# Kernel tuning notes

Hardware: AMD Instinct MI355X
Metric: run time of the kernel (lower is better)

Reference implementation:

```python
import jax, jax.numpy as jnp
import numpy as np

E = 262144      # number of edges / neighbors
F = 128         # scalar feature dim
N_RBF = 20      # radial basis functions
RC = 5.0        # cosine cutoff radius


def setup_inputs() -> dict:
    key = jax.random.key(0)
    ks = jax.random.split(key, 9)
    s = jax.random.normal(ks[0], (E, F), dtype=jnp.float32)
    r = jax.random.normal(ks[1], (E, 3), dtype=jnp.float32)   # displacement vectors, |r|~1.7 < RC
    v = jax.random.normal(ks[2], (E, 3, F), dtype=jnp.float32)
    # learned params (fan-in scaled)
    W1 = jax.random.normal(ks[3], (F, F), dtype=jnp.float32) / np.sqrt(F)
    b1 = jnp.zeros((F,), dtype=jnp.float32)
    W2 = jax.random.normal(ks[4], (F, 3 * F), dtype=jnp.float32) / np.sqrt(F)
    b2 = jnp.zeros((3 * F,), dtype=jnp.float32)
    Wr = jax.random.normal(ks[5], (N_RBF, 3 * F), dtype=jnp.float32) / np.sqrt(N_RBF)
    br = jnp.zeros((3 * F,), dtype=jnp.float32)
    return {"s": s, "r": r, "v": v, "W1": W1, "b1": b1, "W2": W2, "b2": b2, "Wr": Wr, "br": br}


def reference(s, r, v, W1, b1, W2, b2, Wr, br):
    # PaiNN message block: RBF/cutoff-gated projections, hadamard splits, sum over edges.
    d = jnp.linalg.norm(r, axis=-1, keepdims=True)                  # [E,1]
    n = jnp.arange(1, N_RBF + 1, dtype=s.dtype)                     # [20]
    rbf = jnp.sin(n * jnp.pi * d / RC) / d                          # [E,20] sinc radial basis
    fcut = 0.5 * (jnp.cos(jnp.pi * d / RC) + 1.0) * (d < RC)        # [E,1] cosine cutoff
    # filter-generating network on scalar features
    phi = jax.nn.silu(s @ W1 + b1) @ W2 + b2                        # [E,384]
    Wfilt = (rbf @ Wr + br) * fcut                                  # [E,384]
    split = Wfilt * phi                                             # [E,384] hadamard gate
    wv1 = split[:, :F]            # gates existing vector features
    ws = split[:, F:2 * F]        # scalar message
    wv2 = split[:, 2 * F:]        # gates unit direction vectors
    out_s = jnp.sum(ws, axis=0)                                     # [128]
    unit_r = r / d                                                  # [E,3]
    dv = unit_r[:, :, None] * wv2[:, None, :] + wv1[:, None, :] * v # [E,3,128]
    out_v = jnp.sum(dv, axis=0)                                     # [3,128]
    return (out_v, out_s)
```

## Files before the change

kernel.cpp:

```cpp
#include <hip/hip_runtime.h>


#define E_TOT  262144
#define NTILES 16384
#define NBLK   256
#define PART_STRIDE 896

typedef __attribute__((ext_vector_type(8))) short bf16x8;
typedef __attribute__((ext_vector_type(4))) float f32x4;
typedef __attribute__((ext_vector_type(4))) unsigned short u16x4;

static __device__ __forceinline__ unsigned short f2bf(float f) {
  union { float f; unsigned u; } x; x.f = f;
  unsigned r = x.u + 0x7fffu + ((x.u >> 16) & 1u);
  return (unsigned short)(r >> 16);
}
static __device__ __forceinline__ float bf2f(unsigned short h) {
  union { unsigned u; float f; } x; x.u = ((unsigned)h) << 16;
  return x.f;
}

#define BAR() do {                                           \
    asm volatile("s_waitcnt lgkmcnt(0)" ::: "memory");       \
    __builtin_amdgcn_s_barrier();                            \
    asm volatile("" ::: "memory");                           \
  } while (0)

__global__ void prep_kernel(const float* __restrict__ W1, const float* __restrict__ W2,
                            const float* __restrict__ Wr,
                            unsigned short* __restrict__ w1t, unsigned short* __restrict__ w2t,
                            unsigned short* __restrict__ wrt) {
  int idx = blockIdx.x * 256 + threadIdx.x;
  if (idx < 16384) {
    int k = idx >> 7, c = idx & 127;
    float x = W1[idx];
    unsigned short hi = f2bf(x);
    w1t[c * 128 + k] = hi;
    w1t[16384 + c * 128 + k] = f2bf(x - bf2f(hi));
  } else if (idx < 65536) {
    int i = idx - 16384;
    int k = i / 384, c = i % 384;
    float x = W2[i];
    unsigned short hi = f2bf(x);
    w2t[c * 128 + k] = hi;
    w2t[49152 + c * 128 + k] = f2bf(x - bf2f(hi));
  } else if (idx < 77824) {
    int i = idx - 65536;
    int c = i >> 5, n = i & 31;
    float x = (n < 20) ? Wr[n * 384 + c] : 0.0f;
    unsigned short hi = f2bf(x);
    wrt[c * 32 + n] = hi;
    wrt[12288 + c * 32 + n] = f2bf(x - bf2f(hi));
  }
}

__global__ __launch_bounds__(512, 2) void painn_main(
    const float* __restrict__ s, const float* __restrict__ r, const float* __restrict__ v,
    const float* __restrict__ b1, const float* __restrict__ b2, const float* __restrict__ br,
    const unsigned short* __restrict__ w1t, const unsigned short* __restrict__ w2t,
    const unsigned short* __restrict__ wrt, float* __restrict__ partials)
{
  __shared__ __align__(16) unsigned short sAh[16][136], sAl[16][136];
  __shared__ __align__(16) unsigned short hAh[16][136], hAl[16][136];
  __shared__ __align__(16) unsigned short rbfh[16][40], rbfl[16][40];
  __shared__ float urA[2][16][9];

  const int tid = threadIdx.x;
  const int wv  = tid >> 6;
  const int ln  = tid & 63;
  const int l15 = ln & 15;
  const int q4  = ln >> 4;

  for (int i = tid; i < 640; i += 512) ((unsigned short*)rbfh)[i] = 0;
  for (int i = tid; i < 640; i += 512) ((unsigned short*)rbfl)[i] = 0;

  const int jh = wv * 16 + l15;
  bf16x8 w1fh[4], w1fl[4];
#pragma unroll
  for (int ks = 0; ks < 4; ++ks) {
    w1fh[ks] = *(const bf16x8*)(w1t + jh * 128 + ks * 32 + q4 * 8);
    w1fl[ks] = *(const bf16x8*)(w1t + 16384 + jh * 128 + ks * 32 + q4 * 8);
  }
  const float b1v = b1[jh];

  const int fcBase = wv * 3;
  int jg[3]; float b2v[3], brv[3];
  bf16x8 w2fh[3][4], w2fl[3][4], wrfh[3], wrfl[3];
#pragma unroll
  for (int fci = 0; fci < 3; ++fci) {
    const int j = (fcBase + fci) * 16 + l15;
    jg[fci] = j;
    b2v[fci] = b2[j];
    brv[fci] = br[j];
#pragma unroll
    for (int ks = 0; ks < 4; ++ks) {
      w2fh[fci][ks] = *(const bf16x8*)(w2t + j * 128 + ks * 32 + q4 * 8);
      w2fl[fci][ks] = *(const bf16x8*)(w2t + 49152 + j * 128 + ks * 32 + q4 * 8);
    }
    wrfh[fci] = *(const bf16x8*)(wrt + j * 32 + q4 * 8);
    wrfl[fci] = *(const bf16x8*)(wrt + 12288 + j * 32 + q4 * 8);
  }

  float accS[3]     = {0.f, 0.f, 0.f};
  float accV1[3][3] = {{0.f,0.f,0.f},{0.f,0.f,0.f},{0.f,0.f,0.f}};
  float accV2[3][3] = {{0.f,0.f,0.f},{0.f,0.f,0.f},{0.f,0.f,0.f}};
  const f32x4 zero4 = {0.f, 0.f, 0.f, 0.f};

  const int srow = tid >> 5;
  const int sc4  = (tid & 31) * 4;
  float4 pf;
  float prx = 0.f, pry = 0.f, prz = 0.f;
  pf = *(const float4*)(s + (size_t)((size_t)blockIdx.x * 16 + srow) * 128 + sc4);
  if (tid < 16) {
    const float* rp = r + ((size_t)blockIdx.x * 16 + tid) * 3;
    prx = rp[0]; pry = rp[1]; prz = rp[2];
  }

  int p = 0;
  for (int t = blockIdx.x; t < NTILES; t += NBLK, p ^= 1) {
    const int e0 = t * 16;

    {
      float xs0 = pf.x, xs1 = pf.y, xs2 = pf.z, xs3 = pf.w;
      u16x4 vh, vl;
      unsigned short h0 = f2bf(xs0); vh[0] = h0; vl[0] = f2bf(xs0 - bf2f(h0));
      unsigned short h1 = f2bf(xs1); vh[1] = h1; vl[1] = f2bf(xs1 - bf2f(h1));
      unsigned short h2 = f2bf(xs2); vh[2] = h2; vl[2] = f2bf(xs2 - bf2f(h2));
      unsigned short h3 = f2bf(xs3); vh[3] = h3; vl[3] = f2bf(xs3 - bf2f(h3));
      *(u16x4*)&sAh[srow][sc4] = vh;
      *(u16x4*)&sAl[srow][sc4] = vl;
    }
    if (tid < 16) {
      const float x = prx, y = pry, z = prz;
      const float d = sqrtf(x * x + y * y + z * z);
      const float inv = 1.0f / d;
      urA[p][tid][0] = x * inv; urA[p][tid][1] = y * inv; urA[p][tid][2] = z * inv;
      urA[p][tid][3] = (d < 5.0f) ? 0.5f * (cosf(0.62831853071795864f * d) + 1.0f) : 0.0f;
      urA[p][tid][4] = d; urA[p][tid][5] = inv;
    }
    BAR();

    if (tid < 320) {
      const int e_ = tid & 15;
      const int n  = tid >> 4;
      const float d = urA[p][e_][4], inv = urA[p][e_][5];
      const float val = sinf(0.62831853071795864f * (float)(n + 1) * d) * inv;
      const unsigned short hi = f2bf(val);
      rbfh[e_][n] = hi;
      rbfl[e_][n] = f2bf(val - bf2f(hi));
    }

    f32x4 hacc = zero4;
#pragma unroll
    for (int ks = 0; ks < 4; ++ks) {
      const bf16x8 ah = *(const bf16x8*)&sAh[l15][ks * 32 + q4 * 8];
      const bf16x8 al = *(const bf16x8*)&sAl[l15][ks * 32 + q4 * 8];
      hacc = __builtin_amdgcn_mfma_f32_16x16x32_bf16(ah, w1fh[ks], hacc, 0, 0, 0);
      hacc = __builtin_amdgcn_mfma_f32_16x16x32_bf16(al, w1fh[ks], hacc, 0, 0, 0);
      hacc = __builtin_amdgcn_mfma_f32_16x16x32_bf16(ah, w1fl[ks], hacc, 0, 0, 0);
    }
#pragma unroll
    for (int rr = 0; rr < 4; ++rr) {
      const float x = hacc[rr] + b1v;
      const float hvv = x / (1.0f + __expf(-x));
      const unsigned short hi = f2bf(hvv);
      hAh[q4 * 4 + rr][jh] = hi;
      hAl[q4 * 4 + rr][jh] = f2bf(hvv - bf2f(hi));
    }

    {
      int tn = t + NBLK;
      if (tn >= NTILES) tn = blockIdx.x;
      pf = *(const float4*)(s + (size_t)((size_t)tn * 16 + srow) * 128 + sc4);
      if (tid < 16) {
        const float* rp = r + ((size_t)tn * 16 + tid) * 3;
        prx = rp[0]; pry = rp[1]; prz = rp[2];
      }
    }
    BAR();

    f32x4 wacc[3], pacc[3];
    {
      const bf16x8 rh = *(const bf16x8*)&rbfh[l15][q4 * 8];
      const bf16x8 rl = *(const bf16x8*)&rbfl[l15][q4 * 8];
#pragma unroll
      for (int fci = 0; fci < 3; ++fci) {
        f32x4 a = __builtin_amdgcn_mfma_f32_16x16x32_bf16(rh, wrfh[fci], zero4, 0, 0, 0);
        a = __builtin_amdgcn_mfma_f32_16x16x32_bf16(rl, wrfh[fci], a, 0, 0, 0);
        a = __builtin_amdgcn_mfma_f32_16x16x32_bf16(rh, wrfl[fci], a, 0, 0, 0);
        wacc[fci] = a;
        pacc[fci] = zero4;
      }
    }
#pragma unroll
    for (int ks = 0; ks < 4; ++ks) {
      const bf16x8 ah = *(const bf16x8*)&hAh[l15][ks * 32 + q4 * 8];
      const bf16x8 al = *(const bf16x8*)&hAl[l15][ks * 32 + q4 * 8];
#pragma unroll
      for (int fci = 0; fci < 3; ++fci) {
        pacc[fci] = __builtin_amdgcn_mfma_f32_16x16x32_bf16(ah, w2fh[fci][ks], pacc[fci], 0, 0, 0);
        pacc[fci] = __builtin_amdgcn_mfma_f32_16x16x32_bf16(al, w2fh[fci][ks], pacc[fci], 0, 0, 0);
        pacc[fci] = __builtin_amdgcn_mfma_f32_16x16x32_bf16(ah, w2fl[fci][ks], pacc[fci], 0, 0, 0);
      }
    }

#pragma unroll
    for (int fci = 0; fci < 3; ++fci) {
      const int fc = fcBase + fci;
      if (fc < 8) {
        const float* vb = v + (size_t)e0 * 384 + jg[fci];
#pragma unroll
        for (int rr = 0; rr < 4; ++rr) {
          const int el = q4 * 4 + rr;
          const float sp = urA[p][el][3] * (wacc[fci][rr] + brv[fci])
                         * (pacc[fci][rr] + b2v[fci]);
          const float* vp = vb + (size_t)el * 384;
          accV1[fci][0] += sp * vp[0];
          accV1[fci][1] += sp * vp[128];
          accV1[fci][2] += sp * vp[256];
        }
      } else if (fc < 16) {
#pragma unroll
        for (int rr = 0; rr < 4; ++rr) {
          const int el = q4 * 4 + rr;
          accS[fci] += urA[p][el][3] * (wacc[fci][rr] + brv[fci])
                     * (pacc[fci][rr] + b2v[fci]);
        }
      } else {
#pragma unroll
        for (int rr = 0; rr < 4; ++rr) {
          const int el = q4 * 4 + rr;
          const float sp = urA[p][el][3] * (wacc[fci][rr] + brv[fci])
                         * (pacc[fci][rr] + b2v[fci]);
          accV2[fci][0] += urA[p][el][0] * sp;
          accV2[fci][1] += urA[p][el][1] * sp;
          accV2[fci][2] += urA[p][el][2] * sp;
        }
      }
    }
  }

  float* pb = partials + (size_t)blockIdx.x * PART_STRIDE;
#pragma unroll
  for (int fci = 0; fci < 3; ++fci) {
    const int fc = fcBase + fci;
    if (fc < 8) {
#pragma unroll
      for (int c = 0; c < 3; ++c) {
        float tv = accV1[fci][c];
        tv += __shfl_xor(tv, 16);
        tv += __shfl_xor(tv, 32);
        if (ln < 16) pb[c * 128 + jg[fci]] = tv;
      }
    } else if (fc < 16) {
      float tv = accS[fci];
      tv += __shfl_xor(tv, 16);
      tv += __shfl_xor(tv, 32);
      if (ln < 16) pb[768 + (jg[fci] - 128)] = tv;
    } else {
#pragma unroll
      for (int c = 0; c < 3; ++c) {
        float tv = accV2[fci][c];
        tv += __shfl_xor(tv, 16);
        tv += __shfl_xor(tv, 32);
        if (ln < 16) pb[384 + c * 128 + (jg[fci] - 256)] = tv;
      }
    }
  }
}

__global__ void reduce_kernel(const float* __restrict__ partials, float* __restrict__ out) {
  const int o = blockIdx.x * 256 + threadIdx.x;
  float a0 = 0.f, a1 = 0.f, a2 = 0.f, a3 = 0.f;
  if (o < 384) {
#pragma unroll 4
    for (int b = 0; b < NBLK; b += 4) {
      a0 += partials[(size_t)(b + 0) * PART_STRIDE + o] + partials[(size_t)(b + 0) * PART_STRIDE + 384 + o];
      a1 += partials[(size_t)(b + 1) * PART_STRIDE + o] + partials[(size_t)(b + 1) * PART_STRIDE + 384 + o];
      a2 += partials[(size_t)(b + 2) * PART_STRIDE + o] + partials[(size_t)(b + 2) * PART_STRIDE + 384 + o];
      a3 += partials[(size_t)(b + 3) * PART_STRIDE + o] + partials[(size_t)(b + 3) * PART_STRIDE + 384 + o];
    }
    out[o] = (a0 + a1) + (a2 + a3);
  } else {
    const int j = o - 384;
#pragma unroll 4
    for (int b = 0; b < NBLK; b += 4) {
      a0 += partials[(size_t)(b + 0) * PART_STRIDE + 768 + j];
      a1 += partials[(size_t)(b + 1) * PART_STRIDE + 768 + j];
      a2 += partials[(size_t)(b + 2) * PART_STRIDE + 768 + j];
      a3 += partials[(size_t)(b + 3) * PART_STRIDE + 768 + j];
    }
    out[o] = (a0 + a1) + (a2 + a3);
  }
}

extern "C" void kernel_launch(void* const* d_in, const int* in_sizes, int n_in,
                              void* d_out, int out_size, void* d_ws, size_t ws_size,
                              hipStream_t stream) {
  const float* s  = (const float*)d_in[0];
  const float* r  = (const float*)d_in[1];
  const float* v  = (const float*)d_in[2];
  const float* W1 = (const float*)d_in[3];
  const float* b1 = (const float*)d_in[4];
  const float* W2 = (const float*)d_in[5];
  const float* b2 = (const float*)d_in[6];
  const float* Wr = (const float*)d_in[7];
  const float* br = (const float*)d_in[8];
  float* out = (float*)d_out;

  char* ws = (char*)d_ws;
  float* partials = (float*)ws;
  unsigned short* w1t = (unsigned short*)(ws + (size_t)NBLK * PART_STRIDE * 4);
  unsigned short* w2t = w1t + 32768;
  unsigned short* wrt = w2t + 98304;

  prep_kernel<<<304, 256, 0, stream>>>(W1, W2, Wr, w1t, w2t, wrt);
  painn_main<<<NBLK, 512, 0, stream>>>(s, r, v, b1, b2, br, w1t, w2t, wrt, partials);
  reduce_kernel<<<2, 256, 0, stream>>>(partials, out);
}
```

Measured before the change: 837.9 us.

## Rebalance per-wave column mapping, double-buffer RBF, merge barrier, double block count

Each wave now owns the same 16-column slice in all three 128-wide splits (wv1, ws, wv2), so every wave does identical work. Before, some waves handled the vector-gated columns with extra v loads and others did not. The v loads are issued at the start of each tile so their latency overlaps the MFMA work. RBF and cutoff computation are folded into the first barrier phase using double-buffered rbf arrays, which removes one barrier per tile, and unit vectors are packed into a float4. The grid grows to 512 blocks with launch bounds of 4 blocks per CU, which tightens the register budget and may cause spills given the large register-resident weight fragments.

Result: slower. 1.245 ms (+48.6%).

```diff
diff --git a/kernel.cpp b/kernel.cpp
--- a/kernel.cpp
+++ b/kernel.cpp
@@ -3,7 +3,7 @@
 
 #define E_TOT  262144
 #define NTILES 16384
-#define NBLK   256
+#define NBLK   512
 #define PART_STRIDE 896
 
 typedef __attribute__((ext_vector_type(8))) short bf16x8;
@@ -54,7 +54,7 @@
   }
 }
 
-__global__ __launch_bounds__(512, 2) void painn_main(
+__global__ __launch_bounds__(512, 4) void painn_main(
     const float* __restrict__ s, const float* __restrict__ r, const float* __restrict__ v,
     const float* __restrict__ b1, const float* __restrict__ b2, const float* __restrict__ br,
     const unsigned short* __restrict__ w1t, const unsigned short* __restrict__ w2t,
@@ -62,34 +62,34 @@
 {
   __shared__ __align__(16) unsigned short sAh[16][136], sAl[16][136];
   __shared__ __align__(16) unsigned short hAh[16][136], hAl[16][136];
-  __shared__ __align__(16) unsigned short rbfh[16][40], rbfl[16][40];
-  __shared__ float urA[2][16][9];
+  __shared__ __align__(16) unsigned short rbfh[2][16][40], rbfl[2][16][40];
+  __shared__ float4 urA[2][16];
 
   const int tid = threadIdx.x;
   const int wv  = tid >> 6;
   const int ln  = tid & 63;
   const int l15 = ln & 15;
   const int q4  = ln >> 4;
-
-  for (int i = tid; i < 640; i += 512) ((unsigned short*)rbfh)[i] = 0;
-  for (int i = tid; i < 640; i += 512) ((unsigned short*)rbfl)[i] = 0;
-
-  const int jh = wv * 16 + l15;
+  const int jcol = wv * 16 + l15;
+
+  for (int i = tid; i < 2 * 16 * 12; i += 512) {
+    const int b = i / 192, rw = (i / 12) % 16, cc = 20 + (i % 12);
+    rbfh[b][rw][cc] = 0; rbfl[b][rw][cc] = 0;
+  }
+
   bf16x8 w1fh[4], w1fl[4];
 #pragma unroll
   for (int ks = 0; ks < 4; ++ks) {
-    w1fh[ks] = *(const bf16x8*)(w1t + jh * 128 + ks * 32 + q4 * 8);
-    w1fl[ks] = *(const bf16x8*)(w1t + 16384 + jh * 128 + ks * 32 + q4 * 8);
-  }
-  const float b1v = b1[jh];
-
-  const int fcBase = wv * 3;
-  int jg[3]; float b2v[3], brv[3];
+    w1fh[ks] = *(const bf16x8*)(w1t + jcol * 128 + ks * 32 + q4 * 8);
+    w1fl[ks] = *(const bf16x8*)(w1t + 16384 + jcol * 128 + ks * 32 + q4 * 8);
+  }
+  const float b1v = b1[jcol];
+
+  float b2v[3], brv[3];
   bf16x8 w2fh[3][4], w2fl[3][4], wrfh[3], wrfl[3];
 #pragma unroll
   for (int fci = 0; fci < 3; ++fci) {
-    const int j = (fcBase + fci) * 16 + l15;
-    jg[fci] = j;
+    const int j = jcol + fci * 128;
     b2v[fci] = b2[j];
     brv[fci] = br[j];
 #pragma unroll
@@ -101,54 +101,60 @@
     wrfl[fci] = *(const bf16x8*)(wrt + 12288 + j * 32 + q4 * 8);
   }
 
-  float accS[3]     = {0.f, 0.f, 0.f};
-  float accV1[3][3] = {{0.f,0.f,0.f},{0.f,0.f,0.f},{0.f,0.f,0.f}};
-  float accV2[3][3] = {{0.f,0.f,0.f},{0.f,0.f,0.f},{0.f,0.f,0.f}};
+  float accS = 0.f;
+  float accV1[3] = {0.f, 0.f, 0.f};
+  float accV2[3] = {0.f, 0.f, 0.f};
   const f32x4 zero4 = {0.f, 0.f, 0.f, 0.f};
 
   const int srow = tid >> 5;
   const int sc4  = (tid & 31) * 4;
-  float4 pf;
-  float prx = 0.f, pry = 0.f, prz = 0.f;
-  pf = *(const float4*)(s + (size_t)((size_t)blockIdx.x * 16 + srow) * 128 + sc4);
-  if (tid < 16) {
-    const float* rp = r + ((size_t)blockIdx.x * 16 + tid) * 3;
-    prx = rp[0]; pry = rp[1]; prz = rp[2];
+  float4 pf = *(const float4*)(s + (size_t)((size_t)blockIdx.x * 16 + srow) * 128 + sc4);
+  float rx = 0.f, ry = 0.f, rz = 0.f;
+  if (tid < 320) {
+    const float* rp = r + ((size_t)blockIdx.x * 16 + (tid & 15)) * 3;
+    rx = rp[0]; ry = rp[1]; rz = rp[2];
   }
 
   int p = 0;
   for (int t = blockIdx.x; t < NTILES; t += NBLK, p ^= 1) {
     const int e0 = t * 16;
 
+    float vp[4][3];
     {
-      float xs0 = pf.x, xs1 = pf.y, xs2 = pf.z, xs3 = pf.w;
+      const float* vb = v + (size_t)e0 * 384 + jcol;
+#pragma unroll
+      for (int rr = 0; rr < 4; ++rr) {
+        const int el = q4 * 4 + rr;
+#pragma unroll
+        for (int c = 0; c < 3; ++c)
+          vp[rr][c] = vb[(size_t)el * 384 + c * 128];
+      }
+    }
+
+    {
       u16x4 vh, vl;
-      unsigned short h0 = f2bf(xs0); vh[0] = h0; vl[0] = f2bf(xs0 - bf2f(h0));
-      unsigned short h1 = f2bf(xs1); vh[1] = h1; vl[1] = f2bf(xs1 - bf2f(h1));
-      unsigned short h2 = f2bf(xs2); vh[2] = h2; vl[2] = f2bf(xs2 - bf2f(h2));
-      unsigned short h3 = f2bf(xs3); vh[3] = h3; vl[3] = f2bf(xs3 - bf2f(h3));
+      unsigned short h0 = f2bf(pf.x); vh[0] = h0; vl[0] = f2bf(pf.x - bf2f(h0));
+      unsigned short h1 = f2bf(pf.y); vh[1] = h1; vl[1] = f2bf(pf.y - bf2f(h1));
+      unsigned short h2 = f2bf(pf.z); vh[2] = h2; vl[2] = f2bf(pf.z - bf2f(h2));
+      unsigned short h3 = f2bf(pf.w); vh[3] = h3; vl[3] = f2bf(pf.w - bf2f(h3));
       *(u16x4*)&sAh[srow][sc4] = vh;
       *(u16x4*)&sAl[srow][sc4] = vl;
     }
-    if (tid < 16) {
-      const float x = prx, y = pry, z = prz;
-      const float d = sqrtf(x * x + y * y + z * z);
+    if (tid < 320) {
+      const float d = sqrtf(rx * rx + ry * ry + rz * rz);
       const float inv = 1.0f / d;
-      urA[p][tid][0] = x * inv; urA[p][tid][1] = y * inv; urA[p][tid][2] = z * inv;
-      urA[p][tid][3] = (d < 5.0f) ? 0.5f * (cosf(0.62831853071795864f * d) + 1.0f) : 0.0f;
-      urA[p][tid][4] = d; urA[p][tid][5] = inv;
-    }
-    BAR();
-
-    if (tid < 320) {
-      const int e_ = tid & 15;
-      const int n  = tid >> 4;
-      const float d = urA[p][e_][4], inv = urA[p][e_][5];
+      const int n = tid >> 4;
       const float val = sinf(0.62831853071795864f * (float)(n + 1) * d) * inv;
       const unsigned short hi = f2bf(val);
-      rbfh[e_][n] = hi;
-      rbfl[e_][n] = f2bf(val - bf2f(hi));
-    }
+      rbfh[p][tid & 15][n] = hi;
+      rbfl[p][tid & 15][n] = f2bf(val - bf2f(hi));
+      if (tid < 16) {
+        const float fcut = (d < 5.0f) ? 0.5f * (cosf(0.62831853071795864f * d) + 1.0f) : 0.0f;
+        float4 u4; u4.x = rx * inv; u4.y = ry * inv; u4.z = rz * inv; u4.w = fcut;
+        urA[p][tid] = u4;
+      }
+    }
+    BAR();
 
     f32x4 hacc = zero4;
 #pragma unroll
@@ -164,25 +170,25 @@
       const float x = hacc[rr] + b1v;
       const float hvv = x / (1.0f + __expf(-x));
       const unsigned short hi = f2bf(hvv);
-      hAh[q4 * 4 + rr][jh] = hi;
-      hAl[q4 * 4 + rr][jh] = f2bf(hvv - bf2f(hi));
+      hAh[q4 * 4 + rr][jcol] = hi;
+      hAl[q4 * 4 + rr][jcol] = f2bf(hvv - bf2f(hi));
     }
 
     {
       int tn = t + NBLK;
       if (tn >= NTILES) tn = blockIdx.x;
       pf = *(const float4*)(s + (size_t)((size_t)tn * 16 + srow) * 128 + sc4);
-      if (tid < 16) {
-        const float* rp = r + ((size_t)tn * 16 + tid) * 3;
-        prx = rp[0]; pry = rp[1]; prz = rp[2];
+      if (tid < 320) {
+        const float* rp = r + ((size_t)tn * 16 + (tid & 15)) * 3;
+        rx = rp[0]; ry = rp[1]; rz = rp[2];
       }
     }
     BAR();
 
     f32x4 wacc[3], pacc[3];
     {
-      const bf16x8 rh = *(const bf16x8*)&rbfh[l15][q4 * 8];
-      const bf16x8 rl = *(const bf16x8*)&rbfl[l15][q4 * 8];
+      const bf16x8 rh = *(const bf16x8*)&rbfh[p][l15][q4 * 8];
+      const bf16x8 rl = *(const bf16x8*)&rbfl[p][l15][q4 * 8];
 #pragma unroll
       for (int fci = 0; fci < 3; ++fci) {
         f32x4 a = __builtin_amdgcn_mfma_f32_16x16x32_bf16(rh, wrfh[fci], zero4, 0, 0, 0);
@@ -205,67 +211,41 @@
     }
 
 #pragma unroll
-    for (int fci = 0; fci < 3; ++fci) {
-      const int fc = fcBase + fci;
-      if (fc < 8) {
-        const float* vb = v + (size_t)e0 * 384 + jg[fci];
-#pragma unroll
-        for (int rr = 0; rr < 4; ++rr) {
-          const int el = q4 * 4 + rr;
-          const float sp = urA[p][el][3] * (wacc[fci][rr] + brv[fci])
-                         * (pacc[fci][rr] + b2v[fci]);
-          const float* vp = vb + (size_t)el * 384;
-          accV1[fci][0] += sp * vp[0];
-          accV1[fci][1] += sp * vp[128];
-          accV1[fci][2] += sp * vp[256];
-        }
-      } else if (fc < 16) {
-#pragma unroll
-        for (int rr = 0; rr < 4; ++rr) {
-          const int el = q4 * 4 + rr;
-          accS[fci] += urA[p][el][3] * (wacc[fci][rr] + brv[fci])
-                     * (pacc[fci][rr] + b2v[fci]);
-        }
-      } else {
-#pragma unroll
-        for (int rr = 0; rr < 4; ++rr) {
-          const int el = q4 * 4 + rr;
-          const float sp = urA[p][el][3] * (wacc[fci][rr] + brv[fci])
-                         * (pacc[fci][rr] + b2v[fci]);
-          accV2[fci][0] += urA[p][el][0] * sp;
-          accV2[fci][1] += urA[p][el][1] * sp;
-          accV2[fci][2] += urA[p][el][2] * sp;
-        }
-      }
+    for (int rr = 0; rr < 4; ++rr) {
+      const float4 u4 = urA[p][q4 * 4 + rr];
+      const float sp0 = u4.w * (wacc[0][rr] + brv[0]) * (pacc[0][rr] + b2v[0]);
+      const float sp1 = u4.w * (wacc[1][rr] + brv[1]) * (pacc[1][rr] + b2v[1]);
+      const float sp2 = u4.w * (wacc[2][rr] + brv[2]) * (pacc[2][rr] + b2v[2]);
+      accV1[0] += sp0 * vp[rr][0];
+      accV1[1] += sp0 * vp[rr][1];
+      accV1[2] += sp0 * vp[rr][2];
+      accS += sp1;
+      accV2[0] += sp2 * u4.x;
+      accV2[1] += sp2 * u4.y;
+      accV2[2] += sp2 * u4.z;
     }
   }
 
   float* pb = partials + (size_t)blockIdx.x * PART_STRIDE;
 #pragma unroll
-  for (int fci = 0; fci < 3; ++fci) {
-    const int fc = fcBase + fci;
-    if (fc < 8) {
-#pragma unroll
-      for (int c = 0; c < 3; ++c) {
-        float tv = accV1[fci][c];
-        tv += __shfl_xor(tv, 16);
-        tv += __shfl_xor(tv, 32);
-        if (ln < 16) pb[c * 128 + jg[fci]] = tv;
-      }
-    } else if (fc < 16) {
-      float tv = accS[fci];
-      tv += __shfl_xor(tv, 16);
-      tv += __shfl_xor(tv, 32);
-      if (ln < 16) pb[768 + (jg[fci] - 128)] = tv;
-    } else {
-#pragma unroll
-      for (int c = 0; c < 3; ++c) {
-        float tv = accV2[fci][c];
-        tv += __shfl_xor(tv, 16);
-        tv += __shfl_xor(tv, 32);
-        if (ln < 16) pb[384 + c * 128 + (jg[fci] - 256)] = tv;
-      }
-    }
+  for (int c = 0; c < 3; ++c) {
+    float tv = accV1[c];
+    tv += __shfl_xor(tv, 16);
+    tv += __shfl_xor(tv, 32);
+    if (ln < 16) pb[c * 128 + jcol] = tv;
+  }
+  {
+    float tv = accS;
+    tv += __shfl_xor(tv, 16);
+    tv += __shfl_xor(tv, 32);
+    if (ln < 16) pb[768 + jcol] = tv;
+  }
+#pragma unroll
+  for (int c = 0; c < 3; ++c) {
+    float tv = accV2[c];
+    tv += __shfl_xor(tv, 16);
+    tv += __shfl_xor(tv, 32);
+    if (ln < 16) pb[384 + c * 128 + jcol] = tv;
   }
 }
 
```
